# Performance work log

Measured on AMD Instinct MI355X. Metric: run time of the kernel, lower is better.

## Reference

```python
import jax, jax.numpy as jnp
import numpy as np

N, D, E, R = 50000, 128, 640000, 500
BN_EPS = 1e-3  # keras BatchNormalization default
L2_EPS = 1e-12  # tf.nn.l2_normalize default


def setup_inputs() -> dict:
    key = jax.random.key(0)
    ks = jax.random.split(key, 10)
    rows = jnp.sort(jax.random.randint(ks[0], (E,), 0, N, dtype=jnp.int32))
    cols = jax.random.randint(ks[1], (E,), 0, N, dtype=jnp.int32)
    return {
        "x": jax.random.normal(ks[2], (N, D), dtype=jnp.float32),
        "rows": rows,
        "cols": cols,
        "adj_vals": jax.random.uniform(ks[3], (E,), dtype=jnp.float32),
        "rel_ids": jax.random.randint(ks[4], (E,), 0, R, dtype=jnp.int32),
        "gamma1": jnp.ones((D,), jnp.float32),
        "beta1": jnp.zeros((D,), jnp.float32),
        "mean1": jnp.zeros((D,), jnp.float32),
        "var1": jnp.ones((D,), jnp.float32),
        "W1": jax.random.normal(ks[5], (D, D), dtype=jnp.float32) * 0.05,
        "b1": jnp.zeros((D,), jnp.float32),
        "gamma2": jnp.ones((D,), jnp.float32),
        "beta2": jnp.zeros((D,), jnp.float32),
        "mean2": jnp.zeros((D,), jnp.float32),
        "var2": jnp.ones((D,), jnp.float32),
        "relation_coeffs": jax.random.uniform(ks[6], (R,), dtype=jnp.float32),
        "coeff_kernel": jax.random.normal(ks[7], (N, 1), dtype=jnp.float32) * 0.05,
        "Wd": jax.random.normal(ks[8], (D, D), dtype=jnp.float32) * 0.05,
        "bd": jnp.zeros((D,), jnp.float32),
    }


def _bn(h, gamma, beta, mean, var):
    # keras BatchNormalization, inference mode (moving stats)
    return (h - mean) * jax.lax.rsqrt(var + BN_EPS) * gamma + beta


def _spmm(vals, rows, cols, h, n):
    # sparse [n,n] @ dense [n,d]: gather source rows, weight, scatter-add to dest
    return jax.ops.segment_sum(vals[:, None] * h[cols], rows, num_segments=n)


def _l2n(a):
    # tf.nn.l2_normalize(a, axis=1)
    sq = jnp.sum(a * a, axis=1, keepdims=True)
    return a * jax.lax.rsqrt(jnp.maximum(sq, L2_EPS))


def reference(x, rows, cols, adj_vals, rel_ids,
              gamma1, beta1, mean1, var1, W1, b1,
              gamma2, beta2, mean2, var2,
              relation_coeffs, coeff_kernel, Wd, bd):
    n = x.shape[0]
    # ---- agg1: alinet_gcn: tanh(A @ (BN(x) @ W1) + b1) ----
    h = _bn(x, gamma1, beta1, mean1, var1)
    y1 = jnp.tanh(_spmm(adj_vals, rows, cols, h @ W1, n) + b1)
    # ---- agg2: Rgin ----
    h2 = _bn(y1, gamma2, beta2, mean2, var2)
    # relation-weighted edge values: A.values / (rel_coeffs[values] + 1)
    ev = adj_vals / (relation_coeffs[rel_ids] + 1.0)
    agg = _spmm(ev, rows, cols, h2, n)
    self_term = h2 * (coeff_kernel + 1.0)  # CoeffLayer(mul=True)
    y2 = (agg + self_term) @ Wd + bd       # Dense(dim)
    # ---- output: concat of per-layer l2-normalized embeddings, renormalized ----
    y = jnp.concatenate([_l2n(x), _l2n(y1), _l2n(y2)], axis=1)
    return _l2n(y)
```

## Files before the change

kernel.cpp:

```cpp
#include <hip/hip_runtime.h>
#include <math.h>

#define D 128
#define BN_EPS 1e-3f
#define L2_EPS 1e-12f

typedef unsigned int uint;
typedef unsigned short ushort;
typedef __attribute__((ext_vector_type(8))) short bf16x8;
typedef __attribute__((ext_vector_type(4))) float f32x4;

__device__ __forceinline__ ushort f2bf(float f) {
  uint u = __float_as_uint(f);
  uint r = (u + 0x7fffu + ((u >> 16) & 1u)) >> 16;
  return (ushort)r;
}
__device__ __forceinline__ float bflo(uint u) { return __uint_as_float(u << 16); }
__device__ __forceinline__ float bfhi(uint u) { return __uint_as_float(u & 0xffff0000u); }
__device__ __forceinline__ float bf2f(ushort h) { return __uint_as_float(((uint)h) << 16); }

__device__ __forceinline__ void pack_bfrag_block(
    const float* __restrict__ W, const float* __restrict__ gamma,
    const float* __restrict__ var, ushort* __restrict__ Bf, int blk, int tid) {
  int t = blk * 256 + tid;
  int f = t >> 6, lane = t & 63;
  int kc = f >> 3, nt = f & 7, q = lane >> 4, m = lane & 15;
  ushort tmp[8];
#pragma unroll
  for (int j = 0; j < 8; ++j) {
    int k = kc * 32 + q * 8 + j;
    float s = gamma[k] * rsqrtf(var[k] + BN_EPS);
    tmp[j] = f2bf(s * W[k * D + nt * 16 + m]);
  }
  uint4 o;
  o.x = (uint)tmp[0] | ((uint)tmp[1] << 16);
  o.y = (uint)tmp[2] | ((uint)tmp[3] << 16);
  o.z = (uint)tmp[4] | ((uint)tmp[5] << 16);
  o.w = (uint)tmp[6] | ((uint)tmp[7] << 16);
  reinterpret_cast<uint4*>(Bf)[t] = o;
}

__device__ __forceinline__ void bn_bias_block(
    const float* __restrict__ W, const float* __restrict__ gamma,
    const float* __restrict__ beta, const float* __restrict__ mean,
    const float* __restrict__ var, float* __restrict__ outb, int j) {
  float acc = 0.f;
  for (int k = 0; k < D; ++k) {
    float s = gamma[k] * rsqrtf(var[k] + BN_EPS);
    float sh = beta[k] - mean[k] * s;
    acc += sh * W[k * D + j];
  }
  outb[j] = acc;
}

__global__ __launch_bounds__(256) void prep_kernel(
    const float* __restrict__ x, ushort* __restrict__ xbf, int n4,
    const int* __restrict__ rows, int* __restrict__ row_ptr, int n, int e,
    const float* __restrict__ W1, const float* __restrict__ g1,
    const float* __restrict__ v1, ushort* __restrict__ Bf1,
    const float* __restrict__ Wd, const float* __restrict__ g2,
    const float* __restrict__ v2, ushort* __restrict__ Bf2,
    const float* __restrict__ beta1, const float* __restrict__ mean1,
    float* __restrict__ bnb,
    const float* __restrict__ beta2, const float* __restrict__ mean2,
    float* __restrict__ shd,
    const int* __restrict__ cols, const float* __restrict__ adj,
    const int* __restrict__ rel, const float* __restrict__ relc,
    uint2* __restrict__ ew1, uint2* __restrict__ ew2,
    int nbConv, int nbRp) {
  const int b = blockIdx.x, tid = threadIdx.x;
  if (b < nbConv) {
    int i = b * 256 + tid;
    if (i < n4) {
      float4 v = reinterpret_cast<const float4*>(x)[i];
      ushort4 o;
      o.x = f2bf(v.x); o.y = f2bf(v.y); o.z = f2bf(v.z); o.w = f2bf(v.w);
      reinterpret_cast<ushort4*>(xbf)[i] = o;
    }
    return;
  }
  int bb = b - nbConv;
  if (bb < nbRp) {
    int i = bb * 256 + tid;
    if (i <= n) {
      int lo = 0, hi = e;
      while (lo < hi) {
        int mid = (lo + hi) >> 1;
        if (rows[mid] < i) lo = mid + 1; else hi = mid;
      }
      row_ptr[i] = lo;
    }
    return;
  }
  bb -= nbRp;
  if (bb < 8) { pack_bfrag_block(W1, g1, v1, Bf1, bb, tid); return; }
  if (bb < 16) { pack_bfrag_block(Wd, g2, v2, Bf2, bb - 8, tid); return; }
  if (bb == 16) { if (tid < D) bn_bias_block(W1, g1, beta1, mean1, v1, bnb, tid); return; }
  if (bb == 17) { if (tid < D) bn_bias_block(Wd, g2, beta2, mean2, v2, shd, tid); return; }
  int i = (bb - 18) * 256 + tid;
  if (i < e) {
    uint c = (uint)cols[i];
    float a = adj[i];
    ew1[i] = make_uint2(c, __float_as_uint(a));
    float w2 = a / (relc[rel[i]] + 1.0f);
    ew2[i] = make_uint2(c, __float_as_uint(w2));
  } else if (i == e) {
    ew1[i] = make_uint2(0u, 0u);
    ew2[i] = make_uint2(0u, 0u);
  }
}

template <bool SELF>
__global__ __launch_bounds__(256) void spmm4_kernel(
    const ushort* __restrict__ src, const int* __restrict__ row_ptr,
    const uint2* __restrict__ ew, const float* __restrict__ ck,
    ushort* __restrict__ outA, float* __restrict__ rowsum, int n) {
  const int lane = threadIdx.x & 63;
  const int g = lane >> 4, m = lane & 15;
  const int r = blockIdx.x * 16 + (threadIdx.x >> 6) * 4 + g;
  const int rr = r < n ? r : n - 1;
  const int e0 = row_ptr[rr];
  int len = row_ptr[rr + 1] - e0;
  if (r >= n) len = 0;
  int mx = len;
  mx = max(mx, __shfl_xor(mx, 16));
  mx = max(mx, __shfl_xor(mx, 32));
  const int lastOff = len > 0 ? len - 1 : 0;

  const uint4* S4 = reinterpret_cast<const uint4*>(src);
  float acc[8] = {0.f, 0.f, 0.f, 0.f, 0.f, 0.f, 0.f, 0.f};
  float ws = 0.f;

  for (int i = 0; i < mx; i += 4) {
    uint2 md[4];
    uint4 gv[4];
#pragma unroll
    for (int u = 0; u < 4; ++u) {
      int ii = i + u;
      int off = ii < len ? ii : lastOff;
      md[u] = ew[e0 + off];
    }
#pragma unroll
    for (int u = 0; u < 4; ++u) gv[u] = S4[(size_t)md[u].x * 16 + m];
#pragma unroll
    for (int u = 0; u < 4; ++u) {
      float w = (i + u) < len ? __uint_as_float(md[u].y) : 0.f;
      ws += w;
      acc[0] = fmaf(w, bflo(gv[u].x), acc[0]);
      acc[1] = fmaf(w, bfhi(gv[u].x), acc[1]);
      acc[2] = fmaf(w, bflo(gv[u].y), acc[2]);
      acc[3] = fmaf(w, bfhi(gv[u].y), acc[3]);
      acc[4] = fmaf(w, bflo(gv[u].z), acc[4]);
      acc[5] = fmaf(w, bfhi(gv[u].z), acc[5]);
      acc[6] = fmaf(w, bflo(gv[u].w), acc[6]);
      acc[7] = fmaf(w, bfhi(gv[u].w), acc[7]);
    }
  }

  if (r >= n) return;
  if (SELF) {
    uint4 us = S4[(size_t)rr * 16 + m];
    float cp = ck[rr] + 1.0f;
    acc[0] = fmaf(cp, bflo(us.x), acc[0]);
    acc[1] = fmaf(cp, bfhi(us.x), acc[1]);
    acc[2] = fmaf(cp, bflo(us.y), acc[2]);
    acc[3] = fmaf(cp, bfhi(us.y), acc[3]);
    acc[4] = fmaf(cp, bflo(us.z), acc[4]);
    acc[5] = fmaf(cp, bfhi(us.z), acc[5]);
    acc[6] = fmaf(cp, bflo(us.w), acc[6]);
    acc[7] = fmaf(cp, bfhi(us.w), acc[7]);
  }
  uint4 o;
  o.x = (uint)f2bf(acc[0]) | ((uint)f2bf(acc[1]) << 16);
  o.y = (uint)f2bf(acc[2]) | ((uint)f2bf(acc[3]) << 16);
  o.z = (uint)f2bf(acc[4]) | ((uint)f2bf(acc[5]) << 16);
  o.w = (uint)f2bf(acc[6]) | ((uint)f2bf(acc[7]) << 16);
  reinterpret_cast<uint4*>(outA)[(size_t)r * 16 + m] = o;
  if (m == 0) rowsum[r] = ws;
}

__global__ __launch_bounds__(256) void gemm1_mfma_kernel(
    const ushort* __restrict__ A, const ushort* __restrict__ Bf,
    const float* __restrict__ bnb, const float* __restrict__ b1,
    const float* __restrict__ rs1, ushort* __restrict__ y1, int M) {
  const int wave = threadIdx.x >> 6, lane = threadIdx.x & 63;
  const int row0 = blockIdx.x * 64 + wave * 16;
  if (row0 >= M) return;
  const int m = lane & 15, q = lane >> 4;
  const int row = row0 + m;
  const int arow = row < M ? row : M - 1;

  const bf16x8* Av = reinterpret_cast<const bf16x8*>(A);
  const bf16x8* Bv = reinterpret_cast<const bf16x8*>(Bf);

  bf16x8 af[4];
#pragma unroll
  for (int kc = 0; kc < 4; ++kc) af[kc] = Av[(size_t)arow * 16 + kc * 4 + q];

  f32x4 acc[8];
#pragma unroll
  for (int nt = 0; nt < 8; ++nt) acc[nt] = (f32x4){0.f, 0.f, 0.f, 0.f};

#pragma unroll
  for (int kc = 0; kc < 4; ++kc) {
#pragma unroll
    for (int nt = 0; nt < 8; ++nt) {
      bf16x8 b = Bv[(kc * 8 + nt) * 64 + lane];
      acc[nt] = __builtin_amdgcn_mfma_f32_16x16x32_bf16(b, af[kc], acc[nt], 0, 0, 0);
    }
  }

  if (row < M) {
    float rs = rs1[row];
#pragma unroll
    for (int nt = 0; nt < 8; ++nt) {
      const float4 bn = *reinterpret_cast<const float4*>(&bnb[nt * 16 + q * 4]);
      const float4 bb = *reinterpret_cast<const float4*>(&b1[nt * 16 + q * 4]);
      ushort4 o;
      o.x = f2bf(tanhf(acc[nt][0] + rs * bn.x + bb.x));
      o.y = f2bf(tanhf(acc[nt][1] + rs * bn.y + bb.y));
      o.z = f2bf(tanhf(acc[nt][2] + rs * bn.z + bb.z));
      o.w = f2bf(tanhf(acc[nt][3] + rs * bn.w + bb.w));
      *reinterpret_cast<ushort4*>(&y1[(size_t)row * D + nt * 16 + q * 4]) = o;
    }
  }
}

__global__ __launch_bounds__(256) void gemm2_fused_kernel(
    const ushort* __restrict__ A2, const ushort* __restrict__ Bf,
    const float* __restrict__ shd, const float* __restrict__ bd,
    const float* __restrict__ rs2, const float* __restrict__ ck,
    const float* __restrict__ x, const ushort* __restrict__ y1,
    float* __restrict__ out, int M) {
  const int wave = threadIdx.x >> 6, lane = threadIdx.x & 63;
  const int row0 = blockIdx.x * 64 + wave * 16;
  if (row0 >= M) return;
  const int m = lane & 15, q = lane >> 4;
  const int row = row0 + m;
  const int arow = row < M ? row : M - 1;

  const bf16x8* Av = reinterpret_cast<const bf16x8*>(A2);
  const bf16x8* Bv = reinterpret_cast<const bf16x8*>(Bf);

  bf16x8 af[4];
#pragma unroll
  for (int kc = 0; kc < 4; ++kc) af[kc] = Av[(size_t)arow * 16 + kc * 4 + q];

  f32x4 acc[8];
#pragma unroll
  for (int nt = 0; nt < 8; ++nt) acc[nt] = (f32x4){0.f, 0.f, 0.f, 0.f};

#pragma unroll
  for (int kc = 0; kc < 4; ++kc) {
#pragma unroll
    for (int nt = 0; nt < 8; ++nt) {
      bf16x8 b = Bv[(kc * 8 + nt) * 64 + lane];
      acc[nt] = __builtin_amdgcn_mfma_f32_16x16x32_bf16(b, af[kc], acc[nt], 0, 0, 0);
    }
  }

  const float rb = rs2[arow] + ck[arow] + 1.0f;
  float4 xv[8];
  ushort4 y1v[8];
  float s0 = 0.f, s1 = 0.f, s2 = 0.f;
#pragma unroll
  for (int nt = 0; nt < 8; ++nt) {
    const float4 sh = *reinterpret_cast<const float4*>(&shd[nt * 16 + q * 4]);
    const float4 bb = *reinterpret_cast<const float4*>(&bd[nt * 16 + q * 4]);
    acc[nt][0] += rb * sh.x + bb.x;
    acc[nt][1] += rb * sh.y + bb.y;
    acc[nt][2] += rb * sh.z + bb.z;
    acc[nt][3] += rb * sh.w + bb.w;
    s2 += acc[nt][0] * acc[nt][0] + acc[nt][1] * acc[nt][1] +
          acc[nt][2] * acc[nt][2] + acc[nt][3] * acc[nt][3];
    xv[nt] = *reinterpret_cast<const float4*>(&x[(size_t)arow * D + nt * 16 + q * 4]);
    s0 += xv[nt].x * xv[nt].x + xv[nt].y * xv[nt].y +
          xv[nt].z * xv[nt].z + xv[nt].w * xv[nt].w;
    y1v[nt] = *reinterpret_cast<const ushort4*>(&y1[(size_t)arow * D + nt * 16 + q * 4]);
    float ya = bf2f(y1v[nt].x), yb = bf2f(y1v[nt].y);
    float yc = bf2f(y1v[nt].z), yd = bf2f(y1v[nt].w);
    s1 += ya * ya + yb * yb + yc * yc + yd * yd;
  }
  s0 += __shfl_xor(s0, 16); s0 += __shfl_xor(s0, 32);
  s1 += __shfl_xor(s1, 16); s1 += __shfl_xor(s1, 32);
  s2 += __shfl_xor(s2, 16); s2 += __shfl_xor(s2, 32);
  const float i0 = 1.0f / sqrtf(fmaxf(s0, L2_EPS));
  const float i1 = 1.0f / sqrtf(fmaxf(s1, L2_EPS));
  const float i2 = 1.0f / sqrtf(fmaxf(s2, L2_EPS));
  const float tot = s0 * i0 * i0 + s1 * i1 * i1 + s2 * i2 * i2;
  const float sc = 1.0f / sqrtf(fmaxf(tot, L2_EPS));
  const float f0 = i0 * sc, f1 = i1 * sc, f2 = i2 * sc;

  if (row < M) {
    float* orow = out + (size_t)row * 384;
#pragma unroll
    for (int nt = 0; nt < 8; ++nt) {
      const int c = nt * 16 + q * 4;
      float4 ox = make_float4(xv[nt].x * f0, xv[nt].y * f0, xv[nt].z * f0, xv[nt].w * f0);
      float4 oy = make_float4(bf2f(y1v[nt].x) * f1, bf2f(y1v[nt].y) * f1,
                              bf2f(y1v[nt].z) * f1, bf2f(y1v[nt].w) * f1);
      float4 oz = make_float4(acc[nt][0] * f2, acc[nt][1] * f2,
                              acc[nt][2] * f2, acc[nt][3] * f2);
      *reinterpret_cast<float4*>(orow + c) = ox;
      *reinterpret_cast<float4*>(orow + 128 + c) = oy;
      *reinterpret_cast<float4*>(orow + 256 + c) = oz;
    }
  }
}

extern "C" void kernel_launch(void* const* d_in, const int* in_sizes, int n_in,
                              void* d_out, int out_size, void* d_ws, size_t ws_size,
                              hipStream_t stream) {
  const float* x      = (const float*)d_in[0];
  const int*   rows   = (const int*)d_in[1];
  const int*   cols   = (const int*)d_in[2];
  const float* adj    = (const float*)d_in[3];
  const int*   rel    = (const int*)d_in[4];
  const float* gamma1 = (const float*)d_in[5];
  const float* beta1  = (const float*)d_in[6];
  const float* mean1  = (const float*)d_in[7];
  const float* var1   = (const float*)d_in[8];
  const float* W1     = (const float*)d_in[9];
  const float* b1     = (const float*)d_in[10];
  const float* gamma2 = (const float*)d_in[11];
  const float* beta2  = (const float*)d_in[12];
  const float* mean2  = (const float*)d_in[13];
  const float* var2   = (const float*)d_in[14];
  const float* relc   = (const float*)d_in[15];
  const float* ck     = (const float*)d_in[16];
  const float* Wd     = (const float*)d_in[17];
  const float* bd     = (const float*)d_in[18];
  float* out = (float*)d_out;

  const int n = in_sizes[0] / D;
  const int e = in_sizes[1];
  size_t nd = (size_t)n * D;

  char* p = (char*)d_ws;
  ushort* xbf   = (ushort*)p; p += nd * 2;
  ushort* y1bf  = (ushort*)p; p += nd * 2;
  ushort* aggbf = (ushort*)p; p += nd * 2;
  ushort* Bf1   = (ushort*)p; p += 32768;
  ushort* Bf2   = (ushort*)p; p += 32768;
  float*  bnb   = (float*)p;  p += 512;
  float*  shd   = (float*)p;  p += 512;
  float*  rs1   = (float*)p;  p += (size_t)n * 4;
  float*  rs2   = (float*)p;  p += (size_t)n * 4;
  p = (char*)(((uintptr_t)p + 15) & ~(uintptr_t)15);
  uint2* ew1    = (uint2*)p;  p += (size_t)(e + 1) * 8;
  uint2* ew2    = (uint2*)p;  p += (size_t)(e + 1) * 8;
  int* row_ptr  = (int*)p;    p += (size_t)(n + 1) * 4;

  const int n4 = (int)(nd / 4);
  const int nbConv = (n4 + 255) / 256;
  const int nbRp = (n + 1 + 255) / 256;
  const int nbEw = (e + 1 + 255) / 256;
  const int nbPrep = nbConv + nbRp + 18 + nbEw;

  prep_kernel<<<nbPrep, 256, 0, stream>>>(
      x, xbf, n4, rows, row_ptr, n, e,
      W1, gamma1, var1, Bf1, Wd, gamma2, var2, Bf2,
      beta1, mean1, bnb, beta2, mean2, shd,
      cols, adj, rel, relc, ew1, ew2, nbConv, nbRp);

  int sblocks = (n + 15) / 16;
  int gblocks = (n + 63) / 64;

  spmm4_kernel<false><<<sblocks, 256, 0, stream>>>(
      xbf, row_ptr, ew1, nullptr, aggbf, rs1, n);
  gemm1_mfma_kernel<<<gblocks, 256, 0, stream>>>(aggbf, Bf1, bnb, b1, rs1, y1bf, n);
  spmm4_kernel<true><<<sblocks, 256, 0, stream>>>(
      y1bf, row_ptr, ew2, ck, aggbf, rs2, n);
  gemm2_fused_kernel<<<gblocks, 256, 0, stream>>>(
      aggbf, Bf2, shd, bd, rs2, ck, x, y1bf, out, n);
}
```

Before: 229.3 us.

## Fuse SpMM into following MFMA GEMM kernels via shared-memory aggregation tile

Each SpMM stage now runs inside the GEMM kernel: a block aggregates 64 rows into a padded LDS tile (plus row weight sums) and then feeds the MFMA GEMM from LDS. This removes the bf16 aggregation buffer and rowsum round trips through global memory and cuts the launch count from four to two. The edge-metadata loads are also software-pipelined one group of four ahead of the gathers. In exchange, each block serialises four row passes per wave, with fewer blocks and less latency hiding in the gather phase.

```diff
diff --git a/kernel.cpp b/kernel.cpp
--- a/kernel.cpp
+++ b/kernel.cpp
@@ -111,96 +111,109 @@
 }
 
 template <bool SELF>
-__global__ __launch_bounds__(256) void spmm4_kernel(
-    const ushort* __restrict__ src, const int* __restrict__ row_ptr,
+__device__ __forceinline__ void spmm_phase(
+    const uint4* __restrict__ S4, const int* __restrict__ row_ptr,
     const uint2* __restrict__ ew, const float* __restrict__ ck,
-    ushort* __restrict__ outA, float* __restrict__ rowsum, int n) {
+    int n, int blockRow0, uint4* aggL, float* rsL) {
   const int lane = threadIdx.x & 63;
+  const int wave = threadIdx.x >> 6;
   const int g = lane >> 4, m = lane & 15;
-  const int r = blockIdx.x * 16 + (threadIdx.x >> 6) * 4 + g;
-  const int rr = r < n ? r : n - 1;
-  const int e0 = row_ptr[rr];
-  int len = row_ptr[rr + 1] - e0;
-  if (r >= n) len = 0;
-  int mx = len;
-  mx = max(mx, __shfl_xor(mx, 16));
-  mx = max(mx, __shfl_xor(mx, 32));
-  const int lastOff = len > 0 ? len - 1 : 0;
-
-  const uint4* S4 = reinterpret_cast<const uint4*>(src);
-  float acc[8] = {0.f, 0.f, 0.f, 0.f, 0.f, 0.f, 0.f, 0.f};
-  float ws = 0.f;
-
-  for (int i = 0; i < mx; i += 4) {
+#pragma unroll
+  for (int p = 0; p < 4; ++p) {
+    const int rblk = wave * 16 + p * 4 + g;
+    const int r = blockRow0 + rblk;
+    const int rr = r < n ? r : n - 1;
+    const int e0 = row_ptr[rr];
+    int len = row_ptr[rr + 1] - e0;
+    if (r >= n) len = 0;
+    int mx = len;
+    mx = max(mx, __shfl_xor(mx, 16));
+    mx = max(mx, __shfl_xor(mx, 32));
+    const int lastOff = len > 0 ? len - 1 : 0;
+
+    float acc[8] = {0.f, 0.f, 0.f, 0.f, 0.f, 0.f, 0.f, 0.f};
+    float ws = 0.f;
+
     uint2 md[4];
-    uint4 gv[4];
 #pragma unroll
     for (int u = 0; u < 4; ++u) {
-      int ii = i + u;
-      int off = ii < len ? ii : lastOff;
+      int off = u < len ? u : lastOff;
       md[u] = ew[e0 + off];
     }
-#pragma unroll
-    for (int u = 0; u < 4; ++u) gv[u] = S4[(size_t)md[u].x * 16 + m];
-#pragma unroll
-    for (int u = 0; u < 4; ++u) {
-      float w = (i + u) < len ? __uint_as_float(md[u].y) : 0.f;
-      ws += w;
-      acc[0] = fmaf(w, bflo(gv[u].x), acc[0]);
-      acc[1] = fmaf(w, bfhi(gv[u].x), acc[1]);
-      acc[2] = fmaf(w, bflo(gv[u].y), acc[2]);
-      acc[3] = fmaf(w, bfhi(gv[u].y), acc[3]);
-      acc[4] = fmaf(w, bflo(gv[u].z), acc[4]);
-      acc[5] = fmaf(w, bfhi(gv[u].z), acc[5]);
-      acc[6] = fmaf(w, bflo(gv[u].w), acc[6]);
-      acc[7] = fmaf(w, bfhi(gv[u].w), acc[7]);
-    }
-  }
-
-  if (r >= n) return;
-  if (SELF) {
-    uint4 us = S4[(size_t)rr * 16 + m];
-    float cp = ck[rr] + 1.0f;
-    acc[0] = fmaf(cp, bflo(us.x), acc[0]);
-    acc[1] = fmaf(cp, bfhi(us.x), acc[1]);
-    acc[2] = fmaf(cp, bflo(us.y), acc[2]);
-    acc[3] = fmaf(cp, bfhi(us.y), acc[3]);
-    acc[4] = fmaf(cp, bflo(us.z), acc[4]);
-    acc[5] = fmaf(cp, bfhi(us.z), acc[5]);
-    acc[6] = fmaf(cp, bflo(us.w), acc[6]);
-    acc[7] = fmaf(cp, bfhi(us.w), acc[7]);
-  }
-  uint4 o;
-  o.x = (uint)f2bf(acc[0]) | ((uint)f2bf(acc[1]) << 16);
-  o.y = (uint)f2bf(acc[2]) | ((uint)f2bf(acc[3]) << 16);
-  o.z = (uint)f2bf(acc[4]) | ((uint)f2bf(acc[5]) << 16);
-  o.w = (uint)f2bf(acc[6]) | ((uint)f2bf(acc[7]) << 16);
-  reinterpret_cast<uint4*>(outA)[(size_t)r * 16 + m] = o;
-  if (m == 0) rowsum[r] = ws;
-}
-
-__global__ __launch_bounds__(256) void gemm1_mfma_kernel(
-    const ushort* __restrict__ A, const ushort* __restrict__ Bf,
+    for (int i = 0; i < mx; i += 4) {
+      uint4 gv[4];
+#pragma unroll
+      for (int u = 0; u < 4; ++u) gv[u] = S4[(size_t)md[u].x * 16 + m];
+      uint2 mdn[4];
+#pragma unroll
+      for (int u = 0; u < 4; ++u) {
+        int ii = i + 4 + u;
+        int off = ii < len ? ii : lastOff;
+        mdn[u] = ew[e0 + off];
+      }
+#pragma unroll
+      for (int u = 0; u < 4; ++u) {
+        float w = (i + u) < len ? __uint_as_float(md[u].y) : 0.f;
+        ws += w;
+        acc[0] = fmaf(w, bflo(gv[u].x), acc[0]);
+        acc[1] = fmaf(w, bfhi(gv[u].x), acc[1]);
+        acc[2] = fmaf(w, bflo(gv[u].y), acc[2]);
+        acc[3] = fmaf(w, bfhi(gv[u].y), acc[3]);
+        acc[4] = fmaf(w, bflo(gv[u].z), acc[4]);
+        acc[5] = fmaf(w, bfhi(gv[u].z), acc[5]);
+        acc[6] = fmaf(w, bflo(gv[u].w), acc[6]);
+        acc[7] = fmaf(w, bfhi(gv[u].w), acc[7]);
+      }
+#pragma unroll
+      for (int u = 0; u < 4; ++u) md[u] = mdn[u];
+    }
+    if (SELF) {
+      uint4 us = S4[(size_t)rr * 16 + m];
+      float cp = ck[rr] + 1.0f;
+      acc[0] = fmaf(cp, bflo(us.x), acc[0]);
+      acc[1] = fmaf(cp, bfhi(us.x), acc[1]);
+      acc[2] = fmaf(cp, bflo(us.y), acc[2]);
+      acc[3] = fmaf(cp, bfhi(us.y), acc[3]);
+      acc[4] = fmaf(cp, bflo(us.z), acc[4]);
+      acc[5] = fmaf(cp, bfhi(us.z), acc[5]);
+      acc[6] = fmaf(cp, bflo(us.w), acc[6]);
+      acc[7] = fmaf(cp, bfhi(us.w), acc[7]);
+    }
+    uint4 o;
+    o.x = (uint)f2bf(acc[0]) | ((uint)f2bf(acc[1]) << 16);
+    o.y = (uint)f2bf(acc[2]) | ((uint)f2bf(acc[3]) << 16);
+    o.z = (uint)f2bf(acc[4]) | ((uint)f2bf(acc[5]) << 16);
+    o.w = (uint)f2bf(acc[6]) | ((uint)f2bf(acc[7]) << 16);
+    aggL[rblk * 17 + m] = o;
+    if (m == 0) rsL[rblk] = ws;
+  }
+}
+
+__global__ __launch_bounds__(256) void fused1_kernel(
+    const ushort* __restrict__ xbf, const int* __restrict__ row_ptr,
+    const uint2* __restrict__ ew1, const ushort* __restrict__ Bf,
     const float* __restrict__ bnb, const float* __restrict__ b1,
-    const float* __restrict__ rs1, ushort* __restrict__ y1, int M) {
+    ushort* __restrict__ y1, int n) {
+  __shared__ uint4 aggL[64 * 17];
+  __shared__ float rsL[64];
+  const int blockRow0 = blockIdx.x * 64;
+  spmm_phase<false>(reinterpret_cast<const uint4*>(xbf), row_ptr, ew1,
+                    nullptr, n, blockRow0, aggL, rsL);
+  __syncthreads();
+
   const int wave = threadIdx.x >> 6, lane = threadIdx.x & 63;
-  const int row0 = blockIdx.x * 64 + wave * 16;
-  if (row0 >= M) return;
   const int m = lane & 15, q = lane >> 4;
-  const int row = row0 + m;
-  const int arow = row < M ? row : M - 1;
-
-  const bf16x8* Av = reinterpret_cast<const bf16x8*>(A);
+  const int row = blockRow0 + wave * 16 + m;
   const bf16x8* Bv = reinterpret_cast<const bf16x8*>(Bf);
 
   bf16x8 af[4];
 #pragma unroll
-  for (int kc = 0; kc < 4; ++kc) af[kc] = Av[(size_t)arow * 16 + kc * 4 + q];
+  for (int kc = 0; kc < 4; ++kc)
+    af[kc] = *reinterpret_cast<const bf16x8*>(&aggL[(wave * 16 + m) * 17 + kc * 4 + q]);
 
   f32x4 acc[8];
 #pragma unroll
   for (int nt = 0; nt < 8; ++nt) acc[nt] = (f32x4){0.f, 0.f, 0.f, 0.f};
-
 #pragma unroll
   for (int kc = 0; kc < 4; ++kc) {
 #pragma unroll
@@ -210,8 +223,8 @@
     }
   }
 
-  if (row < M) {
-    float rs = rs1[row];
+  if (row < n) {
+    float rs = rsL[wave * 16 + m];
 #pragma unroll
     for (int nt = 0; nt < 8; ++nt) {
       const float4 bn = *reinterpret_cast<const float4*>(&bnb[nt * 16 + q * 4]);
@@ -226,30 +239,33 @@
   }
 }
 
-__global__ __launch_bounds__(256) void gemm2_fused_kernel(
-    const ushort* __restrict__ A2, const ushort* __restrict__ Bf,
-    const float* __restrict__ shd, const float* __restrict__ bd,
-    const float* __restrict__ rs2, const float* __restrict__ ck,
-    const float* __restrict__ x, const ushort* __restrict__ y1,
-    float* __restrict__ out, int M) {
+__global__ __launch_bounds__(256) void fused2_kernel(
+    const ushort* __restrict__ y1, const int* __restrict__ row_ptr,
+    const uint2* __restrict__ ew2, const float* __restrict__ ck,
+    const ushort* __restrict__ Bf, const float* __restrict__ shd,
+    const float* __restrict__ bd, const float* __restrict__ x,
+    float* __restrict__ out, int n) {
+  __shared__ uint4 aggL[64 * 17];
+  __shared__ float rsL[64];
+  const int blockRow0 = blockIdx.x * 64;
+  spmm_phase<true>(reinterpret_cast<const uint4*>(y1), row_ptr, ew2,
+                   ck, n, blockRow0, aggL, rsL);
+  __syncthreads();
+
   const int wave = threadIdx.x >> 6, lane = threadIdx.x & 63;
-  const int row0 = blockIdx.x * 64 + wave * 16;
-  if (row0 >= M) return;
   const int m = lane & 15, q = lane >> 4;
-  const int row = row0 + m;
-  const int arow = row < M ? row : M - 1;
-
-  const bf16x8* Av = reinterpret_cast<const bf16x8*>(A2);
+  const int row = blockRow0 + wave * 16 + m;
+  const int arow = row < n ? row : n - 1;
   const bf16x8* Bv = reinterpret_cast<const bf16x8*>(Bf);
 
   bf16x8 af[4];
 #pragma unroll
-  for (int kc = 0; kc < 4; ++kc) af[kc] = Av[(size_t)arow * 16 + kc * 4 + q];
+  for (int kc = 0; kc < 4; ++kc)
+    af[kc] = *reinterpret_cast<const bf16x8*>(&aggL[(wave * 16 + m) * 17 + kc * 4 + q]);
 
   f32x4 acc[8];
 #pragma unroll
   for (int nt = 0; nt < 8; ++nt) acc[nt] = (f32x4){0.f, 0.f, 0.f, 0.f};
-
 #pragma unroll
   for (int kc = 0; kc < 4; ++kc) {
 #pragma unroll
@@ -259,7 +275,7 @@
     }
   }
 
-  const float rb = rs2[arow] + ck[arow] + 1.0f;
+  const float rb = rsL[wave * 16 + m] + ck[arow] + 1.0f;
   float4 xv[8];
   ushort4 y1v[8];
   float s0 = 0.f, s1 = 0.f, s2 = 0.f;
@@ -291,7 +307,7 @@
   const float sc = 1.0f / sqrtf(fmaxf(tot, L2_EPS));
   const float f0 = i0 * sc, f1 = i1 * sc, f2 = i2 * sc;
 
-  if (row < M) {
+  if (row < n) {
     float* orow = out + (size_t)row * 384;
 #pragma unroll
     for (int nt = 0; nt < 8; ++nt) {
@@ -339,13 +355,10 @@
   char* p = (char*)d_ws;
   ushort* xbf   = (ushort*)p; p += nd * 2;
   ushort* y1bf  = (ushort*)p; p += nd * 2;
-  ushort* aggbf = (ushort*)p; p += nd * 2;
   ushort* Bf1   = (ushort*)p; p += 32768;
   ushort* Bf2   = (ushort*)p; p += 32768;
   float*  bnb   = (float*)p;  p += 512;
   float*  shd   = (float*)p;  p += 512;
-  float*  rs1   = (float*)p;  p += (size_t)n * 4;
-  float*  rs2   = (float*)p;  p += (size_t)n * 4;
   p = (char*)(((uintptr_t)p + 15) & ~(uintptr_t)15);
   uint2* ew1    = (uint2*)p;  p += (size_t)(e + 1) * 8;
   uint2* ew2    = (uint2*)p;  p += (size_t)(e + 1) * 8;
@@ -363,14 +376,9 @@
       beta1, mean1, bnb, beta2, mean2, shd,
       cols, adj, rel, relc, ew1, ew2, nbConv, nbRp);
 
-  int sblocks = (n + 15) / 16;
-  int gblocks = (n + 63) / 64;
-
-  spmm4_kernel<false><<<sblocks, 256, 0, stream>>>(
-      xbf, row_ptr, ew1, nullptr, aggbf, rs1, n);
-  gemm1_mfma_kernel<<<gblocks, 256, 0, stream>>>(aggbf, Bf1, bnb, b1, rs1, y1bf, n);
-  spmm4_kernel<true><<<sblocks, 256, 0, stream>>>(
-      y1bf, row_ptr, ew2, ck, aggbf, rs2, n);
-  gemm2_fused_kernel<<<gblocks, 256, 0, stream>>>(
-      aggbf, Bf2, shd, bd, rs2, ck, x, y1bf, out, n);
-}
+  int fblocks = (n + 63) / 64;
+  fused1_kernel<<<fblocks, 256, 0, stream>>>(
+      xbf, row_ptr, ew1, Bf1, bnb, b1, y1bf, n);
+  fused2_kernel<<<fblocks, 256, 0, stream>>>(
+      y1bf, row_ptr, ew2, ck, Bf2, shd, bd, x, out, n);
+}
```

After: 232.6 us. Within noise of the previous version (+1.4%).
